# Optimization experiments

Measured on AMD Instinct MI355X. Metric: run time of the kernel, lower is better.

## Reference

```python
import jax, jax.numpy as jnp
import numpy as np

VOCAB, TAGS, EDIM, HDIM = 50000, 32, 256, 512
HALF = HDIM // 2
NEG = -10000.0


def _lstm_dir(x, Wih, Whh, b, reverse):
    # x: [B,S,E]; Wih: [4H,E]; Whh: [4H,H]; b: [4H] (b_ih + b_hh fused).
    B = x.shape[0]
    H = Whh.shape[1]

    def cell(carry, xt):
        h, c = carry
        z = xt @ Wih.T + h @ Whh.T + b            # [B,4H], gate order i,f,g,o
        i, f, g, o = jnp.split(z, 4, axis=-1)
        c = jax.nn.sigmoid(f) * c + jax.nn.sigmoid(i) * jnp.tanh(g)
        h = jax.nn.sigmoid(o) * jnp.tanh(c)
        return (h, c), h

    h0 = jnp.zeros((B, H), x.dtype)
    xs = jnp.swapaxes(x, 0, 1)                    # [S,B,E]
    _, hs = jax.lax.scan(cell, (h0, h0), xs, reverse=reverse)
    return jnp.swapaxes(hs, 0, 1)                 # [B,S,H] aligned to input positions


def _viterbi(feats, trans):
    # feats: [B,S,T] emissions; trans[prev, next] as used in the original recursion.
    B, S, T = feats.shape
    v0 = jnp.full((B, T), NEG, feats.dtype).at[:, 0].set(0.0)

    def step(v, feat_t):
        scores = v[:, :, None] + trans[None]      # [B, prev, next]
        best = jnp.max(scores, axis=1)
        bp = jnp.argmax(scores, axis=1)           # [B,T]
        return best + feat_t, bp

    vT, bps = jax.lax.scan(step, v0, jnp.swapaxes(feats, 0, 1))   # bps: [S,B,T]
    term = vT + trans[0][None]                    # terminal uses transitions[0, :]
    best_scores = jnp.max(term, axis=1)           # [B]
    last_tag = jnp.argmax(term, axis=1)           # [B]

    bidx = jnp.arange(B)

    def back(tag, bp):
        return bp[bidx, tag], tag

    tag0, ys = jax.lax.scan(back, last_tag, bps[1:], reverse=True)  # ys[k] = tag at pos k+1
    paths = jnp.concatenate([tag0[:, None], jnp.swapaxes(ys, 0, 1)], axis=1)  # [B,S]
    return paths, best_scores


def setup_inputs() -> dict:
    key = jax.random.key(0)
    ks = jax.random.split(key, 12)
    B, S = 64, 256
    s = 0.05
    trans = jax.random.normal(ks[10], (TAGS, TAGS), jnp.float32)
    trans = trans.at[:, 0].set(NEG).at[0, :].set(NEG)
    return {
        "sentence": jax.random.randint(ks[0], (B, S), 0, VOCAB, jnp.int32),
        "embed": jax.random.normal(ks[1], (VOCAB, EDIM), jnp.float32) * s,
        "Wih_f": jax.random.normal(ks[2], (4 * HALF, EDIM), jnp.float32) * s,
        "Whh_f": jax.random.normal(ks[3], (4 * HALF, HALF), jnp.float32) * s,
        "b_f": jax.random.normal(ks[4], (4 * HALF,), jnp.float32) * s,
        "Wih_b": jax.random.normal(ks[5], (4 * HALF, EDIM), jnp.float32) * s,
        "Whh_b": jax.random.normal(ks[6], (4 * HALF, HALF), jnp.float32) * s,
        "b_b": jax.random.normal(ks[7], (4 * HALF,), jnp.float32) * s,
        "Wout": jax.random.normal(ks[8], (TAGS, HDIM), jnp.float32) * s,
        "bout": jax.random.normal(ks[9], (TAGS,), jnp.float32) * s,
        "trans": trans,
    }


def reference(sentence, embed, Wih_f, Whh_f, b_f, Wih_b, Whh_b, b_b, Wout, bout, trans):
    # Inference path: dropout is identity in eval mode.
    x = embed[sentence]                           # [B,S,E]
    h_f = _lstm_dir(x, Wih_f, Whh_f, b_f, reverse=False)
    h_b = _lstm_dir(x, Wih_b, Whh_b, b_b, reverse=True)
    h = jnp.concatenate([h_f, h_b], axis=-1)      # [B,S,HDIM]
    feats = h @ Wout.T + bout                     # [B,S,TAGS]
    paths, scores = _viterbi(feats, trans)
    return paths, scores
```

## Files before the change

### kernel.cpp

```cpp
#include <hip/hip_runtime.h>
#include <hip/hip_fp16.h>
#include <stdint.h>

typedef float  f32x4  __attribute__((ext_vector_type(4)));
typedef int    i32x4  __attribute__((ext_vector_type(4)));
typedef short  bf16x8 __attribute__((ext_vector_type(8)));
typedef _Float16 h2v  __attribute__((ext_vector_type(2)));

#define NEGV -10000.0f
#define LOG2E 1.442695041f

__device__ __forceinline__ unsigned short f32_to_bf16(float f){
  union { float f; uint32_t u; } v; v.f = f;
  uint32_t u = v.u;
  u += 0x7fffu + ((u >> 16) & 1u);
  return (unsigned short)(u >> 16);
}
__device__ __forceinline__ float bf16_lo(uint32_t u){
  union { uint32_t u; float f; } v; v.u = (u & 0xffffu) << 16; return v.f;
}
__device__ __forceinline__ float bf16_hi(uint32_t u){
  union { uint32_t u; float f; } v; v.u = u & 0xffff0000u; return v.f;
}
__device__ __forceinline__ float fsig(float x){
  return __builtin_amdgcn_rcpf(1.0f + __builtin_exp2f(-LOG2E * x));
}
__device__ __forceinline__ float ftanh_(float x){
  return 1.0f - 2.0f * __builtin_amdgcn_rcpf(1.0f + __builtin_exp2f(2.0f * LOG2E * x));
}
__device__ __forceinline__ uint32_t enc_i8(float x){
  int v = (int)rintf(x * 512.0f);
  v = v > 127 ? 127 : (v < -127 ? -127 : v);
  return (uint32_t)(v & 0xff);
}
__device__ __forceinline__ float fdot2f(uint32_t w, uint32_t h, float acc){
#if __has_builtin(__builtin_amdgcn_fdot2)
  union { uint32_t u; h2v h; } a, b;
  a.u = w; b.u = h;
  return __builtin_amdgcn_fdot2(a.h, b.h, acc, false);
#else
  acc += __half2float(__ushort_as_half((unsigned short)(w & 0xffffu))) *
         __half2float(__ushort_as_half((unsigned short)(h & 0xffffu)));
  acc += __half2float(__ushort_as_half((unsigned short)(w >> 16))) *
         __half2float(__ushort_as_half((unsigned short)(h >> 16)));
  return acc;
#endif
}
__device__ __forceinline__ void wg_barrier_lds(){
  __builtin_amdgcn_s_waitcnt(0xC07F);
  asm volatile("" ::: "memory");
  __builtin_amdgcn_s_barrier();
  asm volatile("" ::: "memory");
}
__device__ __forceinline__ void wave_lds_fence(){
  __builtin_amdgcn_s_waitcnt(0xC07F);
  asm volatile("" ::: "memory");
}
__device__ __forceinline__ float vpack(float sc, int p){
  const int i = (__float_as_int(sc) & 0xFFFFFFE0) | p;
  return __int_as_float(i);
}

__global__ __launch_bounds__(256) void k_quant(
    const float* __restrict__ whh_f, const float* __restrict__ whh_b,
    uint32_t* __restrict__ wq)
{
  const int id  = blockIdx.x * 256 + threadIdx.x;
  const int dir = id >> 16;
  const int rem = id & 0xffff;
  const int np  = rem >> 6;
  const int d   = rem & 63;
  const int u = np >> 2, g = np & 3;
  const float* __restrict__ w = dir ? whh_b : whh_f;
  const float4 v = *(const float4*)(w + (size_t)(g * 256 + u) * 256 + d * 4);
  wq[id] = enc_i8(v.x) | (enc_i8(v.y) << 8) | (enc_i8(v.z) << 16) | (enc_i8(v.w) << 24);
}

__global__ __launch_bounds__(256) void k_xproj(
    const int* __restrict__ sent, const float* __restrict__ embed,
    const float* __restrict__ wih_f, const float* __restrict__ wih_b,
    const float* __restrict__ bias_f, const float* __restrict__ bias_b,
    unsigned short* __restrict__ xp)
{
  __shared__ __align__(16) short At[128 * 32];
  __shared__ __align__(16) short Bt[128 * 32];
  const int bid = blockIdx.x;
  const int tm = bid >> 4;
  const int tn = bid & 15;
  const int dir = tn >> 3;
  const int nloc0 = (tn & 7) * 128;
  const float* __restrict__ wsrc = dir ? wih_b : wih_f;
  const float* __restrict__ bsrc = dir ? bias_b : bias_f;

  const int tid = threadIdx.x;
  const int wv = tid >> 6;
  const int lane = tid & 63;
  const int lr = lane & 15;
  const int lq = lane >> 4;

  const int r  = tid >> 1;
  const int ch = (tid & 1) * 16;

  const int tok = sent[tm * 128 + r];
  const int nprow = nloc0 + r;
  const float* arow = embed + (size_t)tok * 256 + ch;
  const float* brow = wsrc + (size_t)((nprow & 3) * 256 + (nprow >> 2)) * 256 + ch;
  short* at_dst = At + r * 32 + ch;
  short* bt_dst = Bt + r * 32 + ch;

  f32x4 acc[2][8];
  #pragma unroll
  for (int i = 0; i < 2; i++)
    #pragma unroll
    for (int n = 0; n < 8; n++)
      acc[i][n] = (f32x4){0.f, 0.f, 0.f, 0.f};

  for (int k0 = 0; k0 < 256; k0 += 32) {
    #pragma unroll
    for (int qq = 0; qq < 4; qq++) {
      const float4 va = *(const float4*)(arow + k0 + qq * 4);
      const float4 vb = *(const float4*)(brow + k0 + qq * 4);
      short4 sa, sb;
      sa.x = (short)f32_to_bf16(va.x); sa.y = (short)f32_to_bf16(va.y);
      sa.z = (short)f32_to_bf16(va.z); sa.w = (short)f32_to_bf16(va.w);
      sb.x = (short)f32_to_bf16(vb.x); sb.y = (short)f32_to_bf16(vb.y);
      sb.z = (short)f32_to_bf16(vb.z); sb.w = (short)f32_to_bf16(vb.w);
      *(short4*)(at_dst + qq * 4) = sa;
      *(short4*)(bt_dst + qq * 4) = sb;
    }
    __syncthreads();
    bf16x8 bfr[8];
    #pragma unroll
    for (int n = 0; n < 8; n++)
      bfr[n] = *(const bf16x8*)(Bt + (n * 16 + lr) * 32 + lq * 8);
    #pragma unroll
    for (int i = 0; i < 2; i++) {
      const bf16x8 af = *(const bf16x8*)(At + (wv * 32 + i * 16 + lr) * 32 + lq * 8);
      #pragma unroll
      for (int n = 0; n < 8; n++)
        acc[i][n] = __builtin_amdgcn_mfma_f32_16x16x32_bf16(af, bfr[n], acc[i][n], 0, 0, 0);
    }
    __syncthreads();
  }
  #pragma unroll
  for (int i = 0; i < 2; i++) {
    #pragma unroll
    for (int n = 0; n < 8; n++) {
      const int nloc = nloc0 + n * 16 + lr;
      const float bias = bsrc[(nloc & 3) * 256 + (nloc >> 2)];
      #pragma unroll
      for (int rr = 0; rr < 4; rr++) {
        const int m = tm * 128 + wv * 32 + i * 16 + lq * 4 + rr;
        xp[(size_t)m * 2048 + dir * 1024 + nloc] = f32_to_bf16(acc[i][n][rr] + bias);
      }
    }
  }
}

__global__ __launch_bounds__(512, 2) void k_lstm(
    const unsigned short* __restrict__ xp, const uint32_t* __restrict__ wq,
    __half* __restrict__ hout)
{
  __shared__ __align__(16) unsigned char hbuf[2][256];
  const int bid = blockIdx.x;
  const int dir = bid & 1;
  const int b = bid >> 1;
  const int tid = threadIdx.x;
  const int w = tid >> 6;
  const int l = tid & 63;
  const int lr = l & 15;
  const int q = l >> 4;
  const int nio = lr & 7;
  const int u = w * 32 + nio * 4 + q;

  asm volatile("" ::: "v200", "v201", "v202", "v203");

  i32x4 afr[8][4];
  {
    const unsigned char* wb = (const unsigned char*)wq + (size_t)dir * 262144;
    #pragma unroll
    for (int ni = 0; ni < 8; ni++) {
      const unsigned char* rp = wb + (size_t)(w * 128 + ni * 16 + lr) * 256 + q * 16;
      #pragma unroll
      for (int kt = 0; kt < 4; kt++) {
        afr[ni][kt] = *(const i32x4*)(rp + kt * 64);
        asm volatile("" : "+v"(afr[ni][kt].x), "+v"(afr[ni][kt].y),
                          "+v"(afr[ni][kt].z), "+v"(afr[ni][kt].w));
      }
    }
  }
  if (tid < 64) ((uint32_t*)hbuf[0])[tid] = 0;
  float c = 0.0f;
  const i32x4 kz = (i32x4){0, 0, 0, 0};
  const unsigned short* xpo = xp + (size_t)b * (256 * 2048) + dir * 1024
                                 + w * 128 + nio * 16 + q * 4;
  __half* hb = hout + (size_t)b * (256 * 512) + dir * 256 + u;

  uint2 xa, xb;
  {
    const int t0 = dir ? 255 : 0;
    const int t1 = dir ? 254 : 1;
    xa = *(const uint2*)(xpo + (size_t)t0 * 2048);
    xb = *(const uint2*)(xpo + (size_t)t1 * 2048);
  }
  __syncthreads();

#define LSTM_STEP(SS, SRD, SWR, XC)                                          \
  {                                                                          \
    const int t_ = dir ? (255 - (SS)) : (SS);                                \
    i32x4 bfr[4];                                                            \
    _Pragma("unroll")                                                        \
    for (int kt = 0; kt < 4; kt++)                                           \
      bfr[kt] = *(const i32x4*)(&hbuf[SRD][kt * 64 + q * 16]);               \
    i32x4 acc[8];                                                            \
    _Pragma("unroll")                                                        \
    for (int ni = 0; ni < 8; ni++)                                           \
      acc[ni] = __builtin_amdgcn_mfma_i32_16x16x64_i8(                       \
          afr[ni][0], bfr[0], kz, 0, 0, 0);                                  \
    _Pragma("unroll")                                                        \
    for (int kt = 1; kt < 4; kt++)                                           \
      _Pragma("unroll")                                                      \
      for (int ni = 0; ni < 8; ni++)                                         \
        acc[ni] = __builtin_amdgcn_mfma_i32_16x16x64_i8(                     \
            afr[ni][kt], bfr[kt], acc[ni], 0, 0, 0);                         \
    i32x4 zi = acc[0];                                                       \
    _Pragma("unroll")                                                        \
    for (int ni = 1; ni < 8; ni++) {                                         \
      const bool own = (nio == ni);                                          \
      zi.x = own ? acc[ni].x : zi.x;                                         \
      zi.y = own ? acc[ni].y : zi.y;                                         \
      zi.z = own ? acc[ni].z : zi.z;                                         \
      zi.w = own ? acc[ni].w : zi.w;                                         \
    }                                                                        \
    const float SINV = 1.0f / 65536.0f;                                      \
    const float z_i = (float)zi.x * SINV + bf16_lo(XC.x);                    \
    const float z_f = (float)zi.y * SINV + bf16_hi(XC.x);                    \
    const float z_g = (float)zi.z * SINV + bf16_lo(XC.y);                    \
    const float z_o = (float)zi.w * SINV + bf16_hi(XC.y);                    \
    const float ig = fsig(z_i), fg = fsig(z_f);                              \
    const float gg = ftanh_(z_g), og = fsig(z_o);                            \
    c = fg * c + ig * gg;                                                    \
    const float h_ = og * ftanh_(c);                                         \
    {                                   \
      int spf = (SS) + 2; spf = spf > 255 ? 255 : spf;                       \
      const int tpf = dir ? (255 - spf) : spf;                               \
      XC = *(const uint2*)(xpo + (size_t)tpf * 2048);                        \
    }                                                                        \
    if (lr < 8) {                                                            \
      hb[(size_t)t_ * 512] = __float2half(h_);                               \
      int hq = (int)rintf(h_ * 128.0f);                                      \
      hq = hq > 127 ? 127 : (hq < -127 ? -127 : hq);                         \
      hbuf[SWR][u] = (unsigned char)(hq & 0xff);                             \
    }                                                                        \
    wg_barrier_lds();                                                        \
  }

  for (int s = 0; s < 256; s += 2) {
    LSTM_STEP(s,     0, 1, xa)
    LSTM_STEP(s + 1, 1, 0, xb)
  }
#undef LSTM_STEP
}

__global__ __launch_bounds__(256) void k_feats(
    const __half* __restrict__ hg, const float* __restrict__ wout,
    const float* __restrict__ bout, float* __restrict__ feats)
{
  __shared__ __align__(16) uint32_t W2[32 * 260];
  __shared__ float bo[32];
  const int b  = blockIdx.x >> 2;
  const int t0 = (blockIdx.x & 3) * 64;
  const int tid = threadIdx.x;
  #pragma unroll
  for (int i = 0; i < 32; i++) {
    const float2 v = *(const float2*)(wout + (size_t)i * 512 + tid * 2);
    const uint32_t lo = (uint32_t)__half_as_ushort(__float2half(v.x));
    const uint32_t hi = (uint32_t)__half_as_ushort(__float2half(v.y));
    W2[i * 260 + tid] = lo | (hi << 16);
  }
  if (tid < 32) bo[tid] = bout[tid];
  __syncthreads();
  const int n = tid & 31;
  const int tg = tid >> 5;
  const uint32_t* hrow0 = (const uint32_t*)(hg + (size_t)b * (256 * 512));
  float a[8];
  #pragma unroll
  for (int tt = 0; tt < 8; tt++) a[tt] = 0.0f;
  for (int ck = 0; ck < 8; ck++) {
    uint4 wch[8];
    #pragma unroll
    for (int j = 0; j < 8; j++)
      wch[j] = *(const uint4*)(&W2[n * 260 + ck * 32 + j * 4]);
    #pragma unroll
    for (int tt = 0; tt < 8; tt++) {
      const int t = t0 + tg * 8 + tt;
      const uint4* hr = (const uint4*)(hrow0 + t * 256 + ck * 32);
      float acc = a[tt];
      #pragma unroll
      for (int j = 0; j < 8; j++) {
        const uint4 hq = hr[j];
        acc = fdot2f(wch[j].x, hq.x, acc);
        acc = fdot2f(wch[j].y, hq.y, acc);
        acc = fdot2f(wch[j].z, hq.z, acc);
        acc = fdot2f(wch[j].w, hq.w, acc);
      }
      a[tt] = acc;
    }
  }
  #pragma unroll
  for (int tt = 0; tt < 8; tt++) {
    const int t = t0 + tg * 8 + tt;
    feats[((size_t)b * 256 + t) * 32 + n] = bo[n] + a[tt];
  }
}

__global__ __launch_bounds__(64) void k_viterbi(
    const float* __restrict__ feats, const float* __restrict__ trans,
    int* __restrict__ paths, float* __restrict__ scores)
{
  __shared__ __align__(16) float vbuf[32];
  __shared__ unsigned char bp[256][32];
  __shared__ int tags[256];
  const int tid = threadIdx.x;
  const int n = tid & 31;
  const int hf = tid >> 5;
  const int b = blockIdx.x;
  float tcol[16];
  #pragma unroll
  for (int p = 0; p < 16; p++) tcol[p] = trans[(hf * 16 + p) * 32 + n];
  float v = (n == 0) ? -20000.0f : (NEGV - 20000.0f);
  const float* fb = feats + (size_t)b * (256 * 32) + n;
  float xf0 = fb[0], xf1 = fb[32], xf2 = fb[64], xf3 = fb[96];

  for (int t = 0; t < 256; t++) {
    if (hf == 0) vbuf[n] = v;
    wave_lds_fence();
    float g0, g1, g2, g3;
    #define VG(GI, DST)                                                       \
    {                                                                         \
      const float4 q4 = ((const float4*)vbuf)[hf * 4 + GI];                   \
      const int p0 = hf * 16 + GI * 4;                                        \
      const float c0 = vpack(q4.x + tcol[GI * 4 + 0], p0 + 0);                \
      const float c1 = vpack(q4.y + tcol[GI * 4 + 1], p0 + 1);                \
      const float c2 = vpack(q4.z + tcol[GI * 4 + 2], p0 + 2);                \
      const float c3 = vpack(q4.w + tcol[GI * 4 + 3], p0 + 3);                \
      DST = fmaxf(fmaxf(c0, c1), fmaxf(c2, c3));                              \
    }
    VG(0, g0) VG(1, g1) VG(2, g2) VG(3, g3)
    #undef VG
    const float hbest = fmaxf(fmaxf(g0, g1), fmaxf(g2, g3));
    const float other = __shfl_xor(hbest, 32, 64);
    const float best = fmaxf(hbest, other);
    if (hf == 0) bp[t][n] = (unsigned char)(__float_as_int(best) & 31);
    v = best + xf0;
    xf0 = xf1; xf1 = xf2; xf2 = xf3;
    {
      int tp = t + 4; tp = tp > 255 ? 255 : tp;
      xf3 = fb[(size_t)tp * 32];
    }
  }
  if (hf == 0) vbuf[n] = v + tcol[0];
  wave_lds_fence();
  if (tid == 0) {
    float bs = vbuf[0]; int bt = 0;
    #pragma unroll 1
    for (int p = 1; p < 32; p++) {
      if (vbuf[p] > bs) { bs = vbuf[p]; bt = p; }
    }
    scores[b] = bs + 20000.0f;
    int tg = bt;
    tags[255] = tg;
    #pragma unroll 1
    for (int t = 255; t >= 1; t--) {
      tg = bp[t][tg];
      tags[t - 1] = tg;
    }
  }
  wave_lds_fence();
  #pragma unroll
  for (int i = 0; i < 4; i++) {
    const int t = i * 64 + tid;
    paths[(size_t)b * 256 + t] = tags[t];
  }
}

extern "C" void kernel_launch(void* const* d_in, const int* in_sizes, int n_in,
                              void* d_out, int out_size, void* d_ws, size_t ws_size,
                              hipStream_t stream)
{
  (void)in_sizes; (void)n_in; (void)out_size; (void)ws_size;
  const int*   sent  = (const int*)d_in[0];
  const float* embed = (const float*)d_in[1];
  const float* wih_f = (const float*)d_in[2];
  const float* whh_f = (const float*)d_in[3];
  const float* b_f   = (const float*)d_in[4];
  const float* wih_b = (const float*)d_in[5];
  const float* whh_b = (const float*)d_in[6];
  const float* b_b   = (const float*)d_in[7];
  const float* wout  = (const float*)d_in[8];
  const float* bout  = (const float*)d_in[9];
  const float* trans = (const float*)d_in[10];

  char* ws = (char*)d_ws;
  unsigned short* XP = (unsigned short*)(ws);
  __half*   Hg = (__half*)(ws + 67108864);
  uint32_t* WQ = (uint32_t*)(ws + 83886080);
  float*    FT = (float*)(ws + 84410368);

  int*   paths  = (int*)d_out;
  float* scores = (float*)d_out + 16384;

  k_quant  <<<dim3(512),  dim3(256), 0, stream>>>(whh_f, whh_b, WQ);
  k_xproj  <<<dim3(2048), dim3(256), 0, stream>>>(sent, embed, wih_f, wih_b, b_f, b_b, XP);
  k_lstm   <<<dim3(128),  dim3(512), 0, stream>>>(XP, WQ, Hg);
  k_feats  <<<dim3(256),  dim3(256), 0, stream>>>(Hg, wout, bout, FT);
  k_viterbi<<<dim3(64),   dim3(64),  0, stream>>>(FT, trans, paths, scores);
}
```

Baseline: 507.2 us.

## Replace int8 MFMA recurrent matvec with per-lane sdot4 dot products in LSTM

```diff
diff --git a/kernel.cpp b/kernel.cpp
--- a/kernel.cpp
+++ b/kernel.cpp
@@ -3,7 +3,6 @@
 #include <stdint.h>
 
 typedef float  f32x4  __attribute__((ext_vector_type(4)));
-typedef int    i32x4  __attribute__((ext_vector_type(4)));
 typedef short  bf16x8 __attribute__((ext_vector_type(8)));
 typedef _Float16 h2v  __attribute__((ext_vector_type(2)));
 
@@ -32,6 +31,17 @@
   int v = (int)rintf(x * 512.0f);
   v = v > 127 ? 127 : (v < -127 ? -127 : v);
   return (uint32_t)(v & 0xff);
+}
+__device__ __forceinline__ int sdot4(uint32_t a, uint32_t b, int c){
+#if __has_builtin(__builtin_amdgcn_sdot4)
+  return __builtin_amdgcn_sdot4((int)a, (int)b, c, false);
+#else
+  #pragma unroll
+  for (int k = 0; k < 4; k++)
+    c += (int)(signed char)((a >> (8*k)) & 0xff) *
+         (int)(signed char)((b >> (8*k)) & 0xff);
+  return c;
+#endif
 }
 __device__ __forceinline__ float fdot2f(uint32_t w, uint32_t h, float acc){
 #if __has_builtin(__builtin_amdgcn_fdot2)
@@ -168,89 +178,78 @@
   const int tid = threadIdx.x;
   const int w = tid >> 6;
   const int l = tid & 63;
-  const int lr = l & 15;
-  const int q = l >> 4;
-  const int nio = lr & 7;
-  const int u = w * 32 + nio * 4 + q;
-
-  asm volatile("" ::: "v200", "v201", "v202", "v203");
-
-  i32x4 afr[8][4];
+  const int u = w * 32 + (l >> 1);
+  const int role = l & 1;
+
+  uint32_t w0[64], w1[64];
   {
-    const unsigned char* wb = (const unsigned char*)wq + (size_t)dir * 262144;
-    #pragma unroll
-    for (int ni = 0; ni < 8; ni++) {
-      const unsigned char* rp = wb + (size_t)(w * 128 + ni * 16 + lr) * 256 + q * 16;
-      #pragma unroll
-      for (int kt = 0; kt < 4; kt++) {
-        afr[ni][kt] = *(const i32x4*)(rp + kt * 64);
-        asm volatile("" : "+v"(afr[ni][kt].x), "+v"(afr[ni][kt].y),
-                          "+v"(afr[ni][kt].z), "+v"(afr[ni][kt].w));
-      }
+    const uint32_t* rp = wq + dir * 65536 + (size_t)(4 * u + 2 * role) * 64;
+    #pragma unroll
+    for (int j = 0; j < 16; j++) {
+      uint4 q0 = *(const uint4*)(rp + j * 4);
+      uint4 q1 = *(const uint4*)(rp + 64 + j * 4);
+      asm volatile("" : "+v"(q0.x), "+v"(q0.y), "+v"(q0.z), "+v"(q0.w),
+                        "+v"(q1.x), "+v"(q1.y), "+v"(q1.z), "+v"(q1.w));
+      w0[j * 4 + 0] = q0.x; w0[j * 4 + 1] = q0.y;
+      w0[j * 4 + 2] = q0.z; w0[j * 4 + 3] = q0.w;
+      w1[j * 4 + 0] = q1.x; w1[j * 4 + 1] = q1.y;
+      w1[j * 4 + 2] = q1.z; w1[j * 4 + 3] = q1.w;
     }
   }
   if (tid < 64) ((uint32_t*)hbuf[0])[tid] = 0;
   float c = 0.0f;
-  const i32x4 kz = (i32x4){0, 0, 0, 0};
-  const unsigned short* xpo = xp + (size_t)b * (256 * 2048) + dir * 1024
-                                 + w * 128 + nio * 16 + q * 4;
+  const uint32_t* xpd = (const uint32_t*)xp + (size_t)b * (256 * 1024)
+                        + dir * 512 + 2 * u + role;
   __half* hb = hout + (size_t)b * (256 * 512) + dir * 256 + u;
 
-  uint2 xa, xb;
+  uint32_t xa, xb;
   {
     const int t0 = dir ? 255 : 0;
     const int t1 = dir ? 254 : 1;
-    xa = *(const uint2*)(xpo + (size_t)t0 * 2048);
-    xb = *(const uint2*)(xpo + (size_t)t1 * 2048);
+    xa = xpd[(size_t)t0 * 1024];
+    xb = xpd[(size_t)t1 * 1024];
   }
   __syncthreads();
 
 #define LSTM_STEP(SS, SRD, SWR, XC)                                          \
   {                                                                          \
     const int t_ = dir ? (255 - (SS)) : (SS);                                \
-    i32x4 bfr[4];                                                            \
+    const uint4* hb4 = (const uint4*)hbuf[SRD];                              \
+    int a0 = 0, a1 = 0;                                                      \
+    uint4 hc = hb4[0];                                                       \
     _Pragma("unroll")                                                        \
-    for (int kt = 0; kt < 4; kt++)                                           \
-      bfr[kt] = *(const i32x4*)(&hbuf[SRD][kt * 64 + q * 16]);               \
-    i32x4 acc[8];                                                            \
-    _Pragma("unroll")                                                        \
-    for (int ni = 0; ni < 8; ni++)                                           \
-      acc[ni] = __builtin_amdgcn_mfma_i32_16x16x64_i8(                       \
-          afr[ni][0], bfr[0], kz, 0, 0, 0);                                  \
-    _Pragma("unroll")                                                        \
-    for (int kt = 1; kt < 4; kt++)                                           \
-      _Pragma("unroll")                                                      \
-      for (int ni = 0; ni < 8; ni++)                                         \
-        acc[ni] = __builtin_amdgcn_mfma_i32_16x16x64_i8(                     \
-            afr[ni][kt], bfr[kt], acc[ni], 0, 0, 0);                         \
-    i32x4 zi = acc[0];                                                       \
-    _Pragma("unroll")                                                        \
-    for (int ni = 1; ni < 8; ni++) {                                         \
-      const bool own = (nio == ni);                                          \
-      zi.x = own ? acc[ni].x : zi.x;                                         \
-      zi.y = own ? acc[ni].y : zi.y;                                         \
-      zi.z = own ? acc[ni].z : zi.z;                                         \
-      zi.w = own ? acc[ni].w : zi.w;                                         \
+    for (int ck = 0; ck < 16; ck++) {                                        \
+      const uint4 hq = hc;                                                   \
+      if (ck < 15) hc = hb4[ck + 1];                                         \
+      a0 = sdot4(w0[ck * 4 + 0], hq.x, a0);                                  \
+      a0 = sdot4(w0[ck * 4 + 1], hq.y, a0);                                  \
+      a0 = sdot4(w0[ck * 4 + 2], hq.z, a0);                                  \
+      a0 = sdot4(w0[ck * 4 + 3], hq.w, a0);                                  \
+      a1 = sdot4(w1[ck * 4 + 0], hq.x, a1);                                  \
+      a1 = sdot4(w1[ck * 4 + 1], hq.y, a1);                                  \
+      a1 = sdot4(w1[ck * 4 + 2], hq.z, a1);                                  \
+      a1 = sdot4(w1[ck * 4 + 3], hq.w, a1);                                  \
     }                                                                        \
     const float SINV = 1.0f / 65536.0f;                                      \
-    const float z_i = (float)zi.x * SINV + bf16_lo(XC.x);                    \
-    const float z_f = (float)zi.y * SINV + bf16_hi(XC.x);                    \
-    const float z_g = (float)zi.z * SINV + bf16_lo(XC.y);                    \
-    const float z_o = (float)zi.w * SINV + bf16_hi(XC.y);                    \
-    const float ig = fsig(z_i), fg = fsig(z_f);                              \
-    const float gg = ftanh_(z_g), og = fsig(z_o);                            \
-    c = fg * c + ig * gg;                                                    \
-    const float h_ = og * ftanh_(c);                                         \
+    const float z0 = (float)a0 * SINV + bf16_lo(XC);                         \
+    const float z1 = (float)a1 * SINV + bf16_hi(XC);                         \
     {                                   \
       int spf = (SS) + 2; spf = spf > 255 ? 255 : spf;                       \
       const int tpf = dir ? (255 - spf) : spf;                               \
-      XC = *(const uint2*)(xpo + (size_t)tpf * 2048);                        \
+      XC = xpd[(size_t)tpf * 1024];                                          \
     }                                                                        \
-    if (lr < 8) {                                                            \
+            \
+    const float ga = role ? ftanh_(z0) : fsig(z0);                           \
+    const float gb = fsig(z1);                                               \
+    const float gg = __shfl_xor(ga, 1, 64);      \
+    const float og = __shfl_xor(gb, 1, 64);       \
+    if (role == 0) {                                                         \
+      c = gb * c + ga * gg;                                                  \
+      const float h_ = og * ftanh_(c);                                       \
       hb[(size_t)t_ * 512] = __float2half(h_);                               \
-      int hq = (int)rintf(h_ * 128.0f);                                      \
-      hq = hq > 127 ? 127 : (hq < -127 ? -127 : hq);                         \
-      hbuf[SWR][u] = (unsigned char)(hq & 0xff);                             \
+      int hq_ = (int)rintf(h_ * 128.0f);                                     \
+      hq_ = hq_ > 127 ? 127 : (hq_ < -127 ? -127 : hq_);                     \
+      hbuf[SWR][u] = (unsigned char)(hq_ & 0xff);                            \
     }                                                                        \
     wg_barrier_lds();                                                        \
   }
```

New measurement: 526.9 us. 1.04x slower.
